# Performance work log

Hardware: AMD Instinct MI355X
Metric: run time of the kernel (lower is better)

Reference implementation:

```python
import jax, jax.numpy as jnp
import numpy as np

B, T, H, PRED = 16384, 8, 256, 12


def _cell(x, h, c, Wih, Whh, bih, bhh):
    # PyTorch LSTM gate order: i, f, g, o
    g = x @ Wih.T + h @ Whh.T + bih + bhh
    i, f, gg, o = jnp.split(g, 4, axis=-1)
    c = jax.nn.sigmoid(f) * c + jax.nn.sigmoid(i) * jnp.tanh(gg)
    h = jax.nn.sigmoid(o) * jnp.tanh(c)
    return h, c


def _run_seq(x, layers):
    # stacked LSTM over full sequence, zero initial state; x: [B, T, D]
    b = x.shape[0]
    inp = x
    hs, cs = [], []
    for (Wih, Whh, bih, bhh) in layers:
        h0 = jnp.zeros((b, Whh.shape[1]), x.dtype)

        def step(carry, xt, Wih=Wih, Whh=Whh, bih=bih, bhh=bhh):
            h, c = _cell(xt, carry[0], carry[1], Wih, Whh, bih, bhh)
            return (h, c), h

        (h, c), out = jax.lax.scan(step, (h0, h0), jnp.swapaxes(inp, 0, 1))
        inp = jnp.swapaxes(out, 0, 1)
        hs.append(h)
        cs.append(c)
    return inp, jnp.stack(hs), jnp.stack(cs)


def _step_stack(x, hs, cs, layers):
    # single-timestep pass through stacked LSTM; hs/cs: [L, B, H]
    inp = x
    nh, nc = [], []
    for l, (Wih, Whh, bih, bhh) in enumerate(layers):
        h, c = _cell(inp, hs[l], cs[l], Wih, Whh, bih, bhh)
        inp = h
        nh.append(h)
        nc.append(c)
    return inp, jnp.stack(nh), jnp.stack(nc)


def _forward(x, l1_Wih0, l1_Whh0, l1_bih0, l1_bhh0, l1_Wih1, l1_Whh1, l1_bih1, l1_bhh1,
             l2_Wih0, l2_Whh0, l2_bih0, l2_bhh0, l2_Wih1, l2_Whh1, l2_bih1, l2_bhh1,
             fc1_w, fc1_b, fc2_w, fc2_b):
    L1 = [(l1_Wih0, l1_Whh0, l1_bih0, l1_bhh0), (l1_Wih1, l1_Whh1, l1_bih1, l1_bhh1)]
    L2 = [(l2_Wih0, l2_Whh0, l2_bih0, l2_bhh0), (l2_Wih1, l2_Whh1, l2_bih1, l2_bhh1)]
    out1, h1, c1 = _run_seq(x, L1)           # encode observed track
    _, h2, c2 = _run_seq(out1, L2)
    pos = x[:, -1, :]

    def dec(carry, _):
        pos, h1, c1, h2, c2 = carry
        o1, h1, c1 = _step_stack(pos, h1, c1, L1)
        o2, h2, c2 = _step_stack(o1, h2, c2, L2)
        delta = jax.nn.relu(o2 @ fc1_w.T + fc1_b) @ fc2_w.T + fc2_b
        pos = pos + delta
        return (pos, h1, c1, h2, c2), pos

    _, preds = jax.lax.scan(dec, (pos, h1, c1, h2, c2), None, length=PRED)
    return jnp.swapaxes(preds, 0, 1)  # [B, PRED, 2]


def setup_inputs() -> dict:
    key = jax.random.key(0)
    ks = iter(jax.random.split(key, 32))
    s = 1.0 / np.sqrt(H)  # matches PyTorch LSTM/Linear init scale

    def mk(shape):
        return jax.random.uniform(next(ks), shape, jnp.float32, -s, s)

    d = {"x": jax.random.normal(next(ks), (B, T, 2), jnp.float32)}
    for name, in_dim in [("l1", 2), ("l2", H)]:
        for layer in range(2):
            di = in_dim if layer == 0 else H
            d[f"{name}_Wih{layer}"] = mk((4 * H, di))
            d[f"{name}_Whh{layer}"] = mk((4 * H, H))
            d[f"{name}_bih{layer}"] = mk((4 * H,))
            d[f"{name}_bhh{layer}"] = mk((4 * H,))
    d["fc1_w"] = mk((H, H))
    d["fc1_b"] = mk((H,))
    d["fc2_w"] = mk((2, H))
    d["fc2_b"] = mk((2,))
    return d


def reference(x, l1_Wih0, l1_Whh0, l1_bih0, l1_bhh0, l1_Wih1, l1_Whh1, l1_bih1, l1_bhh1,
              l2_Wih0, l2_Whh0, l2_bih0, l2_bhh0, l2_Wih1, l2_Whh1, l2_bih1, l2_bhh1,
              fc1_w, fc1_b, fc2_w, fc2_b):
    return _forward(x, l1_Wih0, l1_Whh0, l1_bih0, l1_bhh0, l1_Wih1, l1_Whh1, l1_bih1, l1_bhh1,
                    l2_Wih0, l2_Whh0, l2_bih0, l2_bhh0, l2_Wih1, l2_Whh1, l2_bih1, l2_bhh1,
                    fc1_w, fc1_b, fc2_w, fc2_b)
```

## Files before the change

kernel.cpp:

```cpp
#include <hip/hip_runtime.h>
#include <stdint.h>

#define Bsz   16384
#define Tseq  8
#define NPRED 12

typedef __attribute__((ext_vector_type(4))) float    f32x4;
typedef _Float16 h16;
typedef __attribute__((ext_vector_type(8))) _Float16 h16x8;

__device__ __forceinline__ float sigf(float x)   { return 1.f / (1.f + __expf(-x)); }
__device__ __forceinline__ float tanh_f(float x) { return 1.f - 2.f / (__expf(2.f * x) + 1.f); }

__device__ __forceinline__ void gload_lds16(const void* g, void* l) {
  __builtin_amdgcn_global_load_lds(
      (const __attribute__((address_space(1))) void*)g,
      (__attribute__((address_space(3))) void*)l, 16, 0, 0);
}

__global__ void zero_r10(f32x4* __restrict__ p, long n4) {
  long i = (long)blockIdx.x * 256 + threadIdx.x;
  f32x4 z; z[0] = 0.f; z[1] = 0.f; z[2] = 0.f; z[3] = 0.f;
  if (i < n4) p[i] = z;
}
__global__ void mark_r10(float* __restrict__ out) {
  if (blockIdx.x == 0 && threadIdx.x < 64) out[threadIdx.x] = 1000.0f;
}
__global__ void seed_r10(float* __restrict__ pos, const float* __restrict__ x) {
  int b = blockIdx.x * 256 + threadIdx.x;
  pos[2 * b]     = x[(size_t)b * 16 + 14];
  pos[2 * b + 1] = x[(size_t)b * 16 + 15];
}

__global__ void pack_w(h16* __restrict__ dst, const float* __restrict__ W0,
                       const float* __restrict__ W1, int ksplit, int Kw, int Np,
                       int gatePack) {
  int idx = blockIdx.x * 256 + threadIdx.x;
  if (idx >= Np * Kw) return;
  int np = idx / Kw, k = idx - np * Kw;
  int n = np;
  if (gatePack) {
    int jb = np >> 7, wc = (np >> 6) & 1, gi = (np >> 4) & 3, jr = np & 15;
    n = gi * 256 + jb * 32 + wc * 16 + jr;
  }
  float w = (k < ksplit) ? W0[(size_t)n * ksplit + k]
                         : W1[(size_t)n * (Kw - ksplit) + (k - ksplit)];
  int KB = Kw >> 6;
  int jb = np >> 7, r = np & 127, kb = k >> 6;
  uint32_t byte = (uint32_t)(jb * KB + kb) * 16384u + (uint32_t)r * 128u
                + ((2u * (uint32_t)(k & 63)) ^ (uint32_t)((r & 7) << 4));
  *(h16*)((char*)dst + byte) = (h16)w;
}

__global__ void add_bias(float* __restrict__ dst, const float* __restrict__ a,
                         const float* __restrict__ b) {
  int i = blockIdx.x * 256 + threadIdx.x;
  if (i < 1024) dst[i] = a[i] + b[i];
}

__device__ __forceinline__ void gemm_core(
    const char* A0, const char* A1, const char* Wp, int KB, int by, int m0,
    char* ldsA, char* ldsB, int tid, f32x4 acc[4][4]) {
  const int wave = tid >> 6, lane = tid & 63;
  const int rowa = tid >> 3;
  const int chb  = (tid & 7) * 16;

#pragma unroll
  for (int m = 0; m < 4; m++)
#pragma unroll
    for (int n = 0; n < 4; n++)
#pragma unroll
      for (int e = 0; e < 4; e++) acc[m][n][e] = 0.f;

  const char* aCur   = A0 + (size_t)(m0 + rowa) * 512 + chb;
  const char* a1Base = A1 + (size_t)(m0 + rowa) * 512 + chb;
  const char* wCur   = Wp + (size_t)by * KB * 16384 + rowa * 128 + chb;

  const int wr = wave >> 1, wc = wave & 1;

  for (int kb = 0; kb < KB; ++kb) {
    if (kb == 4) aCur = a1Base;
#pragma unroll
    for (int it = 0; it < 4; ++it) {
      gload_lds16(aCur + it * 16384, ldsA + it * 4096 + wave * 1024);
      gload_lds16(wCur + it * 4096,  ldsB + it * 4096 + wave * 1024);
    }
    __syncthreads();
#pragma unroll
    for (int kk = 0; kk < 2; ++kk) {
      const int kbyte = kk * 64 + (lane >> 4) * 16;
      h16x8 af[4], bfr[4];
#pragma unroll
      for (int mt = 0; mt < 4; ++mt) {
        int r = wr * 64 + mt * 16 + (lane & 15);
        af[mt] = *(const h16x8*)(ldsA + r * 128 + (kbyte ^ ((r & 7) << 4)));
      }
#pragma unroll
      for (int nt = 0; nt < 4; ++nt) {
        int c = wc * 64 + nt * 16 + (lane & 15);
        bfr[nt] = *(const h16x8*)(ldsB + c * 128 + (kbyte ^ ((c & 7) << 4)));
      }
#pragma unroll
      for (int mt = 0; mt < 4; ++mt)
#pragma unroll
        for (int nt = 0; nt < 4; ++nt)
          acc[mt][nt] = __builtin_amdgcn_mfma_f32_16x16x32_f16(af[mt], bfr[nt], acc[mt][nt], 0, 0, 0);
    }
    __syncthreads();
    aCur += 128;
    wCur += 16384;
  }
}

__device__ __forceinline__ void lstm_epilogue(
    f32x4 acc[4][4], int m0, int n0, int tid, const float* bias,
    const float* wih0, const float* xbase, int xstride, int hasx,
    float* Cst, char* hout) {
  const int wave = tid >> 6, lane = tid & 63;
  const int wr = wave >> 1, wc = wave & 1;
  const int j = (n0 >> 2) + wc * 16 + (lane & 15);
  const float bi = bias[j], bff = bias[256 + j], bg = bias[512 + j], bo = bias[768 + j];
  float wi0 = 0, wi1 = 0, wf0 = 0, wf1 = 0, wg0 = 0, wg1 = 0, wo0 = 0, wo1 = 0;
  if (hasx) {
    wi0 = wih0[2 * j];           wi1 = wih0[2 * j + 1];
    wf0 = wih0[2 * (256 + j)];   wf1 = wih0[2 * (256 + j) + 1];
    wg0 = wih0[2 * (512 + j)];   wg1 = wih0[2 * (512 + j) + 1];
    wo0 = wih0[2 * (768 + j)];   wo1 = wih0[2 * (768 + j) + 1];
  }
#pragma unroll
  for (int mt = 0; mt < 4; ++mt) {
#pragma unroll
    for (int e = 0; e < 4; e++) {
      const int b = m0 + wr * 64 + mt * 16 + (lane >> 4) * 4 + e;
      float vi = acc[mt][0][e] + bi;
      float vf = acc[mt][1][e] + bff;
      float vg = acc[mt][2][e] + bg;
      float vo = acc[mt][3][e] + bo;
      if (hasx) {
        const float x0 = xbase[(size_t)b * xstride];
        const float x1 = xbase[(size_t)b * xstride + 1];
        vi += x0 * wi0 + x1 * wi1;
        vf += x0 * wf0 + x1 * wf1;
        vg += x0 * wg0 + x1 * wg1;
        vo += x0 * wo0 + x1 * wo1;
      }
      const size_t ci = (size_t)b * 256 + j;
      float cn = sigf(vf) * Cst[ci] + sigf(vi) * tanh_f(vg);
      float h  = sigf(vo) * tanh_f(cn);
      Cst[ci] = cn;
      *(h16*)(hout + (size_t)b * 512 + (((unsigned)j * 2) ^ (unsigned)((b & 7) << 4))) = (h16)h;
    }
  }
}

struct CellDesc {
  const char* A0; const char* A1; const char* Wp;
  const float* bias; const float* wih0; const float* xbase;
  float* Cst; char* hout;
  int Kw; int xstride; int hasx;
};
struct Fused4 { CellDesc c[4]; };

__global__ __launch_bounds__(256, 4) void cells_diag(Fused4 args) {
  const int cellid = blockIdx.x >> 10;
  const int lid    = blockIdx.x & 1023;
  const CellDesc d = args.c[cellid];

  __shared__ __align__(16) char lds[32768];
  const int tid = threadIdx.x;

  int swz = (lid & 7) * 128 + (lid >> 3);
  const int by = swz & 7, bx = swz >> 3;
  const int m0 = bx * 128, n0 = by * 128;

  f32x4 acc[4][4];
  gemm_core(d.A0, d.A1, d.Wp, d.Kw >> 6, by, m0, lds, lds + 16384, tid, acc);
  lstm_epilogue(acc, m0, n0, tid, d.bias, d.wih0, d.xbase, d.xstride, d.hasx,
                d.Cst, d.hout);
}

template <int NSEG, int HASX, int LSTM>
__global__ __launch_bounds__(256, 4) void cell_gemm(
    const char* __restrict__ A0, const char* __restrict__ A1,
    const char* __restrict__ Wp, int Kw, int NY,
    const float* __restrict__ bias, const float* __restrict__ wih0,
    const float* __restrict__ xbase, int xstride,
    float* __restrict__ Cst, char* __restrict__ hout) {
  __shared__ __align__(16) char lds[32768];
  const int tid = threadIdx.x;

  int lid = blockIdx.x;
  int chunkv = gridDim.x >> 3;
  int swz = (lid & 7) * chunkv + (lid >> 3);
  const int by = swz % NY, bx = swz / NY;
  const int m0 = bx * 128, n0 = by * 128;

  f32x4 acc[4][4];
  gemm_core(A0, NSEG == 2 ? A1 : A0, Wp, Kw >> 6, by, m0, lds, lds + 16384, tid, acc);

  if constexpr (LSTM) {
    lstm_epilogue(acc, m0, n0, tid, bias, wih0, xbase, xstride, HASX, Cst, hout);
  } else {
    const int wave = tid >> 6, lane = tid & 63;
    const int wr = wave >> 1, wc = wave & 1;
#pragma unroll
    for (int nt = 0; nt < 4; ++nt) {
      const int n = n0 + wc * 64 + nt * 16 + (lane & 15);
      const float bn = bias[n];
#pragma unroll
      for (int mt = 0; mt < 4; ++mt)
#pragma unroll
        for (int e = 0; e < 4; e++) {
          const int b = m0 + wr * 64 + mt * 16 + (lane >> 4) * 4 + e;
          float v = acc[mt][nt][e] + bn;
          v = v > 0.f ? v : 0.f;
          *(h16*)(hout + (size_t)b * 512 + (((unsigned)n * 2) ^ (unsigned)((b & 7) << 4))) = (h16)v;
        }
    }
  }
}

__global__ void fc2_pos(const char* __restrict__ r, const float* __restrict__ w,
                        const float* __restrict__ fb, float* __restrict__ pos,
                        float* __restrict__ out, int s) {
  int b = blockIdx.x * 256 + threadIdx.x;
  float a0 = fb[0], a1 = fb[1];
#pragma unroll
  for (int ch = 0; ch < 32; ch++) {
    h16x8 v = *(const h16x8*)(r + (size_t)b * 512 + (((unsigned)ch * 16) ^ (unsigned)((b & 7) << 4)));
#pragma unroll
    for (int e = 0; e < 8; e++) {
      float rv = (float)v[e];
      int k = ch * 8 + e;
      a0 += rv * w[k];
      a1 += rv * w[256 + k];
    }
  }
  float p0 = pos[2 * b] + a0;
  float p1 = pos[2 * b + 1] + a1;
  pos[2 * b] = p0;
  pos[2 * b + 1] = p1;
  out[(size_t)b * (NPRED * 2) + s * 2]     = p0;
  out[(size_t)b * (NPRED * 2) + s * 2 + 1] = p1;
}

extern "C" void kernel_launch(void* const* d_in, const int* in_sizes, int n_in,
                              void* d_out, int out_size, void* d_ws, size_t ws_size,
                              hipStream_t stream) {
  const float* x      = (const float*)d_in[0];
  const float* Wih[4] = {(const float*)d_in[1], (const float*)d_in[5],
                         (const float*)d_in[9], (const float*)d_in[13]};
  const float* Whh[4] = {(const float*)d_in[2], (const float*)d_in[6],
                         (const float*)d_in[10], (const float*)d_in[14]};
  const float* bih[4] = {(const float*)d_in[3], (const float*)d_in[7],
                         (const float*)d_in[11], (const float*)d_in[15]};
  const float* bhh[4] = {(const float*)d_in[4], (const float*)d_in[8],
                         (const float*)d_in[12], (const float*)d_in[16]};
  const float* fc1_w = (const float*)d_in[17];
  const float* fc1_b = (const float*)d_in[18];
  const float* fc2_w = (const float*)d_in[19];
  const float* fc2_b = (const float*)d_in[20];

  char* ws = (char*)d_ws;
  size_t off = 0;
  auto alloc = [&](size_t bytes) -> char* {
    char* p = ws + off;
    off += (bytes + 255) & ~(size_t)255;
    return p;
  };

  float* Cs[4];
  for (int l = 0; l < 4; l++) Cs[l] = (float*)alloc((size_t)Bsz * 256 * 4);
  char* zeroh = alloc((size_t)Bsz * 512);
  char* h10[2] = {alloc((size_t)Bsz * 512), alloc((size_t)Bsz * 512)};
  char* sl[2]  = {alloc((size_t)Bsz * 512), alloc((size_t)Bsz * 512)};
  char* h20[2] = {alloc((size_t)Bsz * 512), alloc((size_t)Bsz * 512)};
  char* h21[2] = {alloc((size_t)Bsz * 512), alloc((size_t)Bsz * 512)};
  char* rbuf = alloc((size_t)Bsz * 512);
  float* pos = (float*)alloc((size_t)Bsz * 2 * 4);
  float* biasc = (float*)alloc(4 * 1024 * 4);
  h16* wp10 = (h16*)alloc((size_t)1024 * 256 * 2);
  h16* wp[3];
  for (int i = 0; i < 3; i++) wp[i] = (h16*)alloc((size_t)1024 * 512 * 2);
  h16* wpf1 = (h16*)alloc((size_t)256 * 256 * 2);

  if (ws_size < off) {
    mark_r10<<<dim3(1), dim3(64), 0, stream>>>((float*)d_out);
    return;
  }

  {
    long n4 = ((size_t)Bsz * 256 * 4 * 4 + (size_t)Bsz * 512) / 16;
    zero_r10<<<dim3((unsigned)((n4 + 255) / 256)), dim3(256), 0, stream>>>((f32x4*)Cs[0], n4);
  }
  seed_r10<<<dim3(Bsz / 256), dim3(256), 0, stream>>>(pos, x);

  pack_w<<<dim3((1024 * 256 + 255) / 256), dim3(256), 0, stream>>>(wp10, Whh[0], Whh[0], 256, 256, 1024, 1);
  pack_w<<<dim3((1024 * 512 + 255) / 256), dim3(256), 0, stream>>>(wp[0], Wih[1], Whh[1], 256, 512, 1024, 1);
  pack_w<<<dim3((1024 * 512 + 255) / 256), dim3(256), 0, stream>>>(wp[1], Wih[2], Whh[2], 256, 512, 1024, 1);
  pack_w<<<dim3((1024 * 512 + 255) / 256), dim3(256), 0, stream>>>(wp[2], Wih[3], Whh[3], 256, 512, 1024, 1);
  pack_w<<<dim3((256 * 256 + 255) / 256), dim3(256), 0, stream>>>(wpf1, fc1_w, fc1_w, 256, 256, 256, 0);
  for (int l = 0; l < 4; l++)
    add_bias<<<dim3(4), dim3(256), 0, stream>>>(biasc + l * 1024, bih[l], bhh[l]);

  char* hbuf[4][2] = {{h10[0], h10[1]}, {sl[0], sl[1]}, {h20[0], h20[1]}, {h21[0], h21[1]}};
  const h16* wpl[4] = {wp10, wp[0], wp[1], wp[2]};
  for (int d = 0; d <= 10; d++) {
    Fused4 args;
    int nc = 0;
    for (int l = 0; l < 4; l++) {
      int t = d - l;
      if (t < 0 || t >= Tseq) continue;
      CellDesc& cd = args.c[nc++];
      cd.A0 = (l == 0) ? ((t == 0) ? zeroh : hbuf[0][(t - 1) & 1])
                       : hbuf[l - 1][t & 1];
      cd.A1 = (l == 0) ? zeroh
                       : ((t == 0) ? zeroh : hbuf[l][(t - 1) & 1]);
      cd.Wp = (const char*)wpl[l];
      cd.bias = biasc + l * 1024;
      cd.wih0 = (l == 0) ? Wih[0] : nullptr;
      cd.xbase = (l == 0) ? (x + t * 2) : nullptr;
      cd.Cst = Cs[l];
      cd.hout = hbuf[l][t & 1];
      cd.Kw = (l == 0) ? 256 : 512;
      cd.xstride = 16;
      cd.hasx = (l == 0) ? 1 : 0;
    }
    cells_diag<<<dim3(nc * 1024), dim3(256), 0, stream>>>(args);
  }

  for (int s = 0; s < NPRED; s++) {
    int u = Tseq + s, cur = u & 1, prev = cur ^ 1;
    cell_gemm<1, 1, 1><<<dim3(1024), dim3(256), 0, stream>>>(
        h10[prev], zeroh, (const char*)wp10, 256, 8, biasc, Wih[0], pos, 2, Cs[0], h10[cur]);
    cell_gemm<2, 0, 1><<<dim3(1024), dim3(256), 0, stream>>>(
        h10[cur], sl[prev], (const char*)wp[0], 512, 8, biasc + 1024, nullptr, nullptr, 0, Cs[1], sl[cur]);
    cell_gemm<2, 0, 1><<<dim3(1024), dim3(256), 0, stream>>>(
        sl[cur], h20[prev], (const char*)wp[1], 512, 8, biasc + 2048, nullptr, nullptr, 0, Cs[2], h20[cur]);
    cell_gemm<2, 0, 1><<<dim3(1024), dim3(256), 0, stream>>>(
        h20[cur], h21[prev], (const char*)wp[2], 512, 8, biasc + 3072, nullptr, nullptr, 0, Cs[3], h21[cur]);
    cell_gemm<1, 0, 0><<<dim3(256), dim3(256), 0, stream>>>(
        h21[cur], zeroh, (const char*)wpf1, 256, 2, fc1_b, nullptr, nullptr, 0, nullptr, rbuf);
    fc2_pos<<<dim3(Bsz / 256), dim3(256), 0, stream>>>(rbuf, fc2_w, fc2_b, pos, (float*)d_out, s);
  }
}
```

Measured before the change: 2.393 ms.

## Skip zero-state work at t=0 and fuse fc1/fc2 head into one kernel

Removes the zero-initialisation kernel and the zero hidden buffer. The first layer-0 step becomes a pointwise kernel with no GEMM, and first-step cells of the other layers use half the K (input only) and skip the forget-gate cell term. Separately, fc1 GEMM, ReLU and the fc2 projection with the position update are fused into one kernel that stages ReLU output in LDS, removing the rbuf round trip and a launch per prediction step. The fused head uses only 128 blocks, each running two GEMM halves serially, so it has less parallelism than the old 256-block fc1 launch.

Result: no change. 2.353 ms (-1.7%).

```diff
diff --git a/kernel.cpp b/kernel.cpp
--- a/kernel.cpp
+++ b/kernel.cpp
@@ -18,15 +18,10 @@
       (__attribute__((address_space(3))) void*)l, 16, 0, 0);
 }
 
-__global__ void zero_r10(f32x4* __restrict__ p, long n4) {
-  long i = (long)blockIdx.x * 256 + threadIdx.x;
-  f32x4 z; z[0] = 0.f; z[1] = 0.f; z[2] = 0.f; z[3] = 0.f;
-  if (i < n4) p[i] = z;
-}
-__global__ void mark_r10(float* __restrict__ out) {
+__global__ void mark_r11(float* __restrict__ out) {
   if (blockIdx.x == 0 && threadIdx.x < 64) out[threadIdx.x] = 1000.0f;
 }
-__global__ void seed_r10(float* __restrict__ pos, const float* __restrict__ x) {
+__global__ void seed_r11(float* __restrict__ pos, const float* __restrict__ x) {
   int b = blockIdx.x * 256 + threadIdx.x;
   pos[2 * b]     = x[(size_t)b * 16 + 14];
   pos[2 * b + 1] = x[(size_t)b * 16 + 15];
@@ -58,6 +53,28 @@
   if (i < 1024) dst[i] = a[i] + b[i];
 }
 
+__global__ void l0t0_pw(const float* __restrict__ x, const float* __restrict__ wih0,
+                        const float* __restrict__ bias, float* __restrict__ Cst,
+                        char* __restrict__ hout) {
+  int gid = blockIdx.x * 256 + threadIdx.x;
+  int b = gid >> 5, jb = (gid & 31) << 3;
+  float x0 = x[(size_t)b * 16], x1 = x[(size_t)b * 16 + 1];
+  float c[8]; h16 hh[8];
+#pragma unroll
+  for (int q = 0; q < 8; ++q) {
+    int j = jb + q;
+    float vi = bias[j]       + x0 * wih0[2 * j]           + x1 * wih0[2 * j + 1];
+    float vg = bias[512 + j] + x0 * wih0[2 * (512 + j)]   + x1 * wih0[2 * (512 + j) + 1];
+    float vo = bias[768 + j] + x0 * wih0[2 * (768 + j)]   + x1 * wih0[2 * (768 + j) + 1];
+    float cn = sigf(vi) * tanh_f(vg);
+    hh[q] = (h16)(sigf(vo) * tanh_f(cn));
+    c[q] = cn;
+  }
+  *(f32x4*)(Cst + (size_t)b * 256 + jb)     = *(f32x4*)c;
+  *(f32x4*)(Cst + (size_t)b * 256 + jb + 4) = *(f32x4*)(c + 4);
+  *(h16x8*)(hout + (size_t)b * 512 + (((unsigned)jb * 2) ^ (unsigned)((b & 7) << 4))) = *(h16x8*)hh;
+}
+
 __device__ __forceinline__ void gemm_core(
     const char* A0, const char* A1, const char* Wp, int KB, int by, int m0,
     char* ldsA, char* ldsB, int tid, f32x4 acc[4][4]) {
@@ -114,7 +131,7 @@
 
 __device__ __forceinline__ void lstm_epilogue(
     f32x4 acc[4][4], int m0, int n0, int tid, const float* bias,
-    const float* wih0, const float* xbase, int xstride, int hasx,
+    const float* wih0, const float* xbase, int xstride, int hasx, int skipc,
     float* Cst, char* hout) {
   const int wave = tid >> 6, lane = tid & 63;
   const int wr = wave >> 1, wc = wave & 1;
@@ -145,8 +162,9 @@
         vo += x0 * wo0 + x1 * wo1;
       }
       const size_t ci = (size_t)b * 256 + j;
-      float cn = sigf(vf) * Cst[ci] + sigf(vi) * tanh_f(vg);
-      float h  = sigf(vo) * tanh_f(cn);
+      float cn = sigf(vi) * tanh_f(vg);
+      if (!skipc) cn += sigf(vf) * Cst[ci];
+      float h = sigf(vo) * tanh_f(cn);
       Cst[ci] = cn;
       *(h16*)(hout + (size_t)b * 512 + (((unsigned)j * 2) ^ (unsigned)((b & 7) << 4))) = (h16)h;
     }
@@ -157,7 +175,7 @@
   const char* A0; const char* A1; const char* Wp;
   const float* bias; const float* wih0; const float* xbase;
   float* Cst; char* hout;
-  int Kw; int xstride; int hasx;
+  int Kw; int xstride; int hasx; int skipc;
 };
 struct Fused4 { CellDesc c[4]; };
 
@@ -176,13 +194,13 @@
   f32x4 acc[4][4];
   gemm_core(d.A0, d.A1, d.Wp, d.Kw >> 6, by, m0, lds, lds + 16384, tid, acc);
   lstm_epilogue(acc, m0, n0, tid, d.bias, d.wih0, d.xbase, d.xstride, d.hasx,
-                d.Cst, d.hout);
-}
-
-template <int NSEG, int HASX, int LSTM>
+                d.skipc, d.Cst, d.hout);
+}
+
+template <int NSEG, int HASX>
 __global__ __launch_bounds__(256, 4) void cell_gemm(
     const char* __restrict__ A0, const char* __restrict__ A1,
-    const char* __restrict__ Wp, int Kw, int NY,
+    const char* __restrict__ Wp, int Kw,
     const float* __restrict__ bias, const float* __restrict__ wih0,
     const float* __restrict__ xbase, int xstride,
     float* __restrict__ Cst, char* __restrict__ hout) {
@@ -192,56 +210,56 @@
   int lid = blockIdx.x;
   int chunkv = gridDim.x >> 3;
   int swz = (lid & 7) * chunkv + (lid >> 3);
-  const int by = swz % NY, bx = swz / NY;
+  const int by = swz % 8, bx = swz / 8;
   const int m0 = bx * 128, n0 = by * 128;
 
   f32x4 acc[4][4];
   gemm_core(A0, NSEG == 2 ? A1 : A0, Wp, Kw >> 6, by, m0, lds, lds + 16384, tid, acc);
-
-  if constexpr (LSTM) {
-    lstm_epilogue(acc, m0, n0, tid, bias, wih0, xbase, xstride, HASX, Cst, hout);
-  } else {
-    const int wave = tid >> 6, lane = tid & 63;
-    const int wr = wave >> 1, wc = wave & 1;
+  lstm_epilogue(acc, m0, n0, tid, bias, wih0, xbase, xstride, HASX, 0, Cst, hout);
+}
+
+__global__ __launch_bounds__(256) void fc_head(
+    const char* __restrict__ A, const char* __restrict__ Wp,
+    const float* __restrict__ b1, const float* __restrict__ w2,
+    const float* __restrict__ b2, float* __restrict__ pos,
+    float* __restrict__ out, int s) {
+  __shared__ __align__(16) char lds[34304];
+  const int tid = threadIdx.x;
+  const int m0 = blockIdx.x * 128;
+  const int wave = tid >> 6, lane = tid & 63;
+  const int wr = wave >> 1, wc = wave & 1;
+  const int bl2 = tid >> 1, comp = tid & 1;
+
+  float a = 0.f;
+  for (int half = 0; half < 2; ++half) {
+    f32x4 acc[4][4];
+    gemm_core(A, A, Wp, 4, half, m0, lds, lds + 16384, tid, acc);
+    h16* strip = (h16*)lds;
 #pragma unroll
     for (int nt = 0; nt < 4; ++nt) {
-      const int n = n0 + wc * 64 + nt * 16 + (lane & 15);
-      const float bn = bias[n];
+      const int n = half * 128 + wc * 64 + nt * 16 + (lane & 15);
+      const int nl = wc * 64 + nt * 16 + (lane & 15);
+      const float bn = b1[n];
 #pragma unroll
       for (int mt = 0; mt < 4; ++mt)
 #pragma unroll
         for (int e = 0; e < 4; e++) {
-          const int b = m0 + wr * 64 + mt * 16 + (lane >> 4) * 4 + e;
+          const int bl = wr * 64 + mt * 16 + (lane >> 4) * 4 + e;
           float v = acc[mt][nt][e] + bn;
-          v = v > 0.f ? v : 0.f;
-          *(h16*)(hout + (size_t)b * 512 + (((unsigned)n * 2) ^ (unsigned)((b & 7) << 4))) = (h16)v;
+          strip[bl * 134 + nl] = (h16)(v > 0.f ? v : 0.f);
         }
     }
-  }
-}
-
-__global__ void fc2_pos(const char* __restrict__ r, const float* __restrict__ w,
-                        const float* __restrict__ fb, float* __restrict__ pos,
-                        float* __restrict__ out, int s) {
-  int b = blockIdx.x * 256 + threadIdx.x;
-  float a0 = fb[0], a1 = fb[1];
-#pragma unroll
-  for (int ch = 0; ch < 32; ch++) {
-    h16x8 v = *(const h16x8*)(r + (size_t)b * 512 + (((unsigned)ch * 16) ^ (unsigned)((b & 7) << 4)));
-#pragma unroll
-    for (int e = 0; e < 8; e++) {
-      float rv = (float)v[e];
-      int k = ch * 8 + e;
-      a0 += rv * w[k];
-      a1 += rv * w[256 + k];
-    }
-  }
-  float p0 = pos[2 * b] + a0;
-  float p1 = pos[2 * b + 1] + a1;
-  pos[2 * b] = p0;
-  pos[2 * b + 1] = p1;
-  out[(size_t)b * (NPRED * 2) + s * 2]     = p0;
-  out[(size_t)b * (NPRED * 2) + s * 2 + 1] = p1;
+    __syncthreads();
+    const float* wrow = w2 + comp * 256 + half * 128;
+#pragma unroll 8
+    for (int n = 0; n < 128; ++n)
+      a += (float)strip[bl2 * 134 + n] * wrow[n];
+    __syncthreads();
+  }
+  const size_t b = (size_t)(m0 + bl2);
+  float p = pos[2 * b + comp] + a + b2[comp];
+  pos[2 * b + comp] = p;
+  out[b * (NPRED * 2) + s * 2 + comp] = p;
 }
 
 extern "C" void kernel_launch(void* const* d_in, const int* in_sizes, int n_in,
@@ -271,12 +289,10 @@
 
   float* Cs[4];
   for (int l = 0; l < 4; l++) Cs[l] = (float*)alloc((size_t)Bsz * 256 * 4);
-  char* zeroh = alloc((size_t)Bsz * 512);
   char* h10[2] = {alloc((size_t)Bsz * 512), alloc((size_t)Bsz * 512)};
   char* sl[2]  = {alloc((size_t)Bsz * 512), alloc((size_t)Bsz * 512)};
   char* h20[2] = {alloc((size_t)Bsz * 512), alloc((size_t)Bsz * 512)};
   char* h21[2] = {alloc((size_t)Bsz * 512), alloc((size_t)Bsz * 512)};
-  char* rbuf = alloc((size_t)Bsz * 512);
   float* pos = (float*)alloc((size_t)Bsz * 2 * 4);
   float* biasc = (float*)alloc(4 * 1024 * 4);
   h16* wp10 = (h16*)alloc((size_t)1024 * 256 * 2);
@@ -285,15 +301,11 @@
   h16* wpf1 = (h16*)alloc((size_t)256 * 256 * 2);
 
   if (ws_size < off) {
-    mark_r10<<<dim3(1), dim3(64), 0, stream>>>((float*)d_out);
+    mark_r11<<<dim3(1), dim3(64), 0, stream>>>((float*)d_out);
     return;
   }
 
-  {
-    long n4 = ((size_t)Bsz * 256 * 4 * 4 + (size_t)Bsz * 512) / 16;
-    zero_r10<<<dim3((unsigned)((n4 + 255) / 256)), dim3(256), 0, stream>>>((f32x4*)Cs[0], n4);
-  }
-  seed_r10<<<dim3(Bsz / 256), dim3(256), 0, stream>>>(pos, x);
+  seed_r11<<<dim3(Bsz / 256), dim3(256), 0, stream>>>(pos, x);
 
   pack_w<<<dim3((1024 * 256 + 255) / 256), dim3(256), 0, stream>>>(wp10, Whh[0], Whh[0], 256, 256, 1024, 1);
   pack_w<<<dim3((1024 * 512 + 255) / 256), dim3(256), 0, stream>>>(wp[0], Wih[1], Whh[1], 256, 512, 1024, 1);
@@ -306,41 +318,43 @@
   char* hbuf[4][2] = {{h10[0], h10[1]}, {sl[0], sl[1]}, {h20[0], h20[1]}, {h21[0], h21[1]}};
   const h16* wpl[4] = {wp10, wp[0], wp[1], wp[2]};
   for (int d = 0; d <= 10; d++) {
+    if (d == 0) {
+      l0t0_pw<<<dim3(2048), dim3(256), 0, stream>>>(x, Wih[0], biasc, Cs[0], hbuf[0][0]);
+      continue;
+    }
     Fused4 args;
     int nc = 0;
     for (int l = 0; l < 4; l++) {
       int t = d - l;
       if (t < 0 || t >= Tseq) continue;
       CellDesc& cd = args.c[nc++];
-      cd.A0 = (l == 0) ? ((t == 0) ? zeroh : hbuf[0][(t - 1) & 1])
-                       : hbuf[l - 1][t & 1];
-      cd.A1 = (l == 0) ? zeroh
-                       : ((t == 0) ? zeroh : hbuf[l][(t - 1) & 1]);
+      cd.A0 = (l == 0) ? hbuf[0][(t - 1) & 1] : hbuf[l - 1][t & 1];
+      cd.A1 = (l > 0 && t > 0) ? hbuf[l][(t - 1) & 1] : cd.A0;
       cd.Wp = (const char*)wpl[l];
       cd.bias = biasc + l * 1024;
       cd.wih0 = (l == 0) ? Wih[0] : nullptr;
       cd.xbase = (l == 0) ? (x + t * 2) : nullptr;
       cd.Cst = Cs[l];
       cd.hout = hbuf[l][t & 1];
-      cd.Kw = (l == 0) ? 256 : 512;
+      cd.Kw = (l == 0 || t == 0) ? 256 : 512;
       cd.xstride = 16;
       cd.hasx = (l == 0) ? 1 : 0;
+      cd.skipc = (t == 0) ? 1 : 0;
     }
     cells_diag<<<dim3(nc * 1024), dim3(256), 0, stream>>>(args);
   }
 
   for (int s = 0; s < NPRED; s++) {
     int u = Tseq + s, cur = u & 1, prev = cur ^ 1;
-    cell_gemm<1, 1, 1><<<dim3(1024), dim3(256), 0, stream>>>(
-        h10[prev], zeroh, (const char*)wp10, 256, 8, biasc, Wih[0], pos, 2, Cs[0], h10[cur]);
-    cell_gemm<2, 0, 1><<<dim3(1024), dim3(256), 0, stream>>>(
-        h10[cur], sl[prev], (const char*)wp[0], 512, 8, biasc + 1024, nullptr, nullptr, 0, Cs[1], sl[cur]);
-    cell_gemm<2, 0, 1><<<dim3(1024), dim3(256), 0, stream>>>(
-        sl[cur], h20[prev], (const char*)wp[1], 512, 8, biasc + 2048, nullptr, nullptr, 0, Cs[2], h20[cur]);
-    cell_gemm<2, 0, 1><<<dim3(1024), dim3(256), 0, stream>>>(
-        h20[cur], h21[prev], (const char*)wp[2], 512, 8, biasc + 3072, nullptr, nullptr, 0, Cs[3], h21[cur]);
-    cell_gemm<1, 0, 0><<<dim3(256), dim3(256), 0, stream>>>(
-        h21[cur], zeroh, (const char*)wpf1, 256, 2, fc1_b, nullptr, nullptr, 0, nullptr, rbuf);
-    fc2_pos<<<dim3(Bsz / 256), dim3(256), 0, stream>>>(rbuf, fc2_w, fc2_b, pos, (float*)d_out, s);
-  }
-}
+    cell_gemm<1, 1><<<dim3(1024), dim3(256), 0, stream>>>(
+        h10[prev], h10[prev], (const char*)wp10, 256, biasc, Wih[0], pos, 2, Cs[0], h10[cur]);
+    cell_gemm<2, 0><<<dim3(1024), dim3(256), 0, stream>>>(
+        h10[cur], sl[prev], (const char*)wp[0], 512, biasc + 1024, nullptr, nullptr, 0, Cs[1], sl[cur]);
+    cell_gemm<2, 0><<<dim3(1024), dim3(256), 0, stream>>>(
+        sl[cur], h20[prev], (const char*)wp[1], 512, biasc + 2048, nullptr, nullptr, 0, Cs[2], h20[cur]);
+    cell_gemm<2, 0><<<dim3(1024), dim3(256), 0, stream>>>(
+        h20[cur], h21[prev], (const char*)wp[2], 512, biasc + 3072, nullptr, nullptr, 0, Cs[3], h21[cur]);
+    fc_head<<<dim3(128), dim3(256), 0, stream>>>(
+        h21[cur], (const char*)wpf1, fc1_b, fc2_w, fc2_b, pos, (float*)d_out, s);
+  }
+}
```
